# Optimization experiments

Hardware: AMD Instinct MI355X
Metric: run time of the kernel (lower is better)

Reference implementation:

```python
import jax, jax.numpy as jnp
import numpy as np

B, T, I, H = 2048, 1024, 1, 64


def setup_inputs() -> dict:
    key = jax.random.key(0)
    ks = jax.random.split(key, 7)
    s = 1.0 / np.sqrt(H)
    return {
        "x": jax.random.normal(ks[0], (B, T, I), dtype=jnp.float32),
        "W_ih": jax.random.uniform(ks[1], (H, I), jnp.float32, -s, s),
        "W_hh": jax.random.uniform(ks[2], (H, H), jnp.float32, -s, s),
        "b_ih": jax.random.uniform(ks[3], (H,), jnp.float32, -s, s),
        "b_hh": jax.random.uniform(ks[4], (H,), jnp.float32, -s, s),
        "W_out": jax.random.uniform(ks[5], (1, H), jnp.float32, -s, s),
        "b_out": jax.random.uniform(ks[6], (1,), jnp.float32, -s, s),
    }


def reference(x, W_ih, W_hh, b_ih, b_hh, W_out, b_out):
    # x: [B, T, I] -> time-major [T, B, I]
    xt = jnp.swapaxes(x, 0, 1)
    # precompute input projection for all timesteps: [T, B, H]
    xp = jnp.einsum('tbi,hi->tbh', xt, W_ih) + b_ih + b_hh
    h0 = jnp.zeros((x.shape[0], W_hh.shape[0]), dtype=x.dtype)

    def step(h, xp_t):
        h_new = jnp.tanh(xp_t + h @ W_hh.T)
        return h_new, None

    h_last, _ = jax.lax.scan(step, h0, xp)
    # final linear + sigmoid on last timestep: [B, 1]
    return jax.nn.sigmoid(h_last @ W_out.T + b_out)
```

## Files before the change

kernel.cpp:

```cpp
#include <hip/hip_runtime.h>


constexpr int T_STEPS = 1024;
constexpr int H = 64;

typedef float v2f __attribute__((ext_vector_type(2)));
typedef float v4f __attribute__((ext_vector_type(4)));

__device__ __forceinline__ float dpp_rotfwd_add(float t, float a) {
    int y = __builtin_amdgcn_mov_dpp(__builtin_bit_cast(int, t), 0x39, 0xF, 0xF, true);
    return __builtin_bit_cast(float, y) + a;
}

__device__ __forceinline__ float tanh_fast(float s) {
    const float e = __builtin_amdgcn_exp2f(s * 2.88539008177792681472f);
    return 1.f - 2.f * __builtin_amdgcn_rcpf(e + 1.f);
}

__global__
__attribute__((amdgpu_flat_work_group_size(64, 64), amdgpu_waves_per_eu(2, 2)))
void rnn_fused(
    const float* __restrict__ x,
    const float* __restrict__ W_ih,
    const float* __restrict__ W_hh,
    const float* __restrict__ b_ih,
    const float* __restrict__ b_hh,
    const float* __restrict__ W_out,
    const float* __restrict__ b_out,
    float* __restrict__ out)
{
    const int b    = blockIdx.x;
    const int lane = threadIdx.x;
    const int og   = lane >> 2;
    const int kg   = lane & 3;

    __shared__ v4f xs4[T_STEPS / 4];
    __shared__ v4f hA4[H / 4];
    __shared__ v4f hB4[H / 4];

    const v4f* xrow = reinterpret_cast<const v4f*>(x + (size_t)b * T_STEPS);
    #pragma unroll
    for (int k = 0; k < T_STEPS / 4 / 64; ++k)
        xs4[lane + 64 * k] = xrow[lane + 64 * k];

    v2f w2[4][8];
    #pragma unroll
    for (int r = 0; r < 4; ++r) {
        const int row = 4 * og + ((kg + r) & 3);
        const float* src = W_hh + (size_t)row * H + 16 * kg;
        #pragma unroll
        for (int c2 = 0; c2 < 8; ++c2)
            w2[r][c2] = *reinterpret_cast<const v2f*>(src + 2 * c2);
    }
    #pragma unroll
    for (int r = 0; r < 4; ++r)
        #pragma unroll
        for (int c2 = 0; c2 < 8; ++c2)
            asm volatile("" : "+v"(w2[r][c2]));

    const float wih  = W_ih[lane];
    const float bias = b_ih[lane] + b_hh[lane];
    const float wout = W_out[lane];

    reinterpret_cast<float*>(hA4)[lane] = 0.f;

    float hn = 0.f;

    auto step = [&](float xv, const v4f* __restrict__ hr,
                    float* __restrict__ hw) {
        const v4f* h4 = hr + 4 * kg;
        v2f accL[4], accM[4];
        accL[0] = v2f{fmaf(xv, wih, bias), 0.f};
        accL[1] = v2f{0.f, 0.f}; accL[2] = v2f{0.f, 0.f}; accL[3] = v2f{0.f, 0.f};
        accM[0] = v2f{0.f, 0.f}; accM[1] = v2f{0.f, 0.f};
        accM[2] = v2f{0.f, 0.f}; accM[3] = v2f{0.f, 0.f};
        #pragma unroll
        for (int c = 0; c < 4; ++c) {
            const v4f hv = h4[c];
            const v2f hlo = __builtin_shufflevector(hv, hv, 0, 1);
            const v2f hhi = __builtin_shufflevector(hv, hv, 2, 3);
            #pragma unroll
            for (int r = 0; r < 4; ++r) {
                accL[r] = __builtin_elementwise_fma(hlo, w2[r][2 * c],     accL[r]);
                accM[r] = __builtin_elementwise_fma(hhi, w2[r][2 * c + 1], accM[r]);
            }
        }
        float a[4];
        #pragma unroll
        for (int r = 0; r < 4; ++r) {
            const v2f s2 = accL[r] + accM[r];
            a[r] = s2.x + s2.y;
        }
        float t = a[1];
        t = dpp_rotfwd_add(t, a[2]);
        t = dpp_rotfwd_add(t, a[3]);
        t = dpp_rotfwd_add(t, a[0]);
        hn = tanh_fast(t);
        hw[lane] = hn;
    };

    #pragma unroll 1
    for (int t4 = 0; t4 < T_STEPS / 4; ++t4) {
        const v4f xq = xs4[t4];
        step(xq.x, hA4, reinterpret_cast<float*>(hB4));
        step(xq.y, hB4, reinterpret_cast<float*>(hA4));
        step(xq.z, hA4, reinterpret_cast<float*>(hB4));
        step(xq.w, hB4, reinterpret_cast<float*>(hA4));
    }

    float p = hn * wout;
    #pragma unroll
    for (int off = 1; off <= 32; off <<= 1)
        p += __shfl_xor(p, off);
    if (lane == 0)
        out[b] = 1.f / (1.f + __expf(-(p + b_out[0])));
}

extern "C" void kernel_launch(void* const* d_in, const int* in_sizes, int n_in,
                              void* d_out, int out_size, void* d_ws, size_t ws_size,
                              hipStream_t stream)
{
    const float* x     = (const float*)d_in[0];
    const float* W_ih  = (const float*)d_in[1];
    const float* W_hh  = (const float*)d_in[2];
    const float* b_ih  = (const float*)d_in[3];
    const float* b_hh  = (const float*)d_in[4];
    const float* W_out = (const float*)d_in[5];
    const float* b_out = (const float*)d_in[6];
    float* out = (float*)d_out;

    const int B = out_size;
    rnn_fused<<<B, 64, 0, stream>>>(x, W_ih, W_hh, b_ih, b_hh, W_out, b_out, out);
}
```

Baseline: 234.5 us.

## Interleave two independent batch rows per wave to hide recurrence latency

Each 64-lane workgroup now runs two batch sequences, alternating their timesteps, and the grid is halved. Because the two recurrences are independent, one sequence's LDS reads, FMAs, DPP reduction and tanh can overlap the other's dependency chain. Occupancy is lowered to one wave per EU, and the first FMA round is peeled so it starts from multiplies instead of zeroed accumulators. The trade-off is fewer waves to hide latency and an assumption that B is even.

Result: slower. 256.9 us (+9.5%).

```diff
diff --git a/kernel.cpp b/kernel.cpp
--- a/kernel.cpp
+++ b/kernel.cpp
@@ -17,8 +17,11 @@
     return 1.f - 2.f * __builtin_amdgcn_rcpf(e + 1.f);
 }
 
+__device__ __forceinline__ v2f vlo(v4f v) { return __builtin_shufflevector(v, v, 0, 1); }
+__device__ __forceinline__ v2f vhi(v4f v) { return __builtin_shufflevector(v, v, 2, 3); }
+
 __global__
-__attribute__((amdgpu_flat_work_group_size(64, 64), amdgpu_waves_per_eu(2, 2)))
+__attribute__((amdgpu_flat_work_group_size(64, 64), amdgpu_waves_per_eu(1, 1)))
 void rnn_fused(
     const float* __restrict__ x,
     const float* __restrict__ W_ih,
@@ -29,19 +32,23 @@
     const float* __restrict__ b_out,
     float* __restrict__ out)
 {
-    const int b    = blockIdx.x;
+    const int bid  = blockIdx.x;
     const int lane = threadIdx.x;
     const int og   = lane >> 2;
     const int kg   = lane & 3;
 
-    __shared__ v4f xs4[T_STEPS / 4];
-    __shared__ v4f hA4[H / 4];
-    __shared__ v4f hB4[H / 4];
+    __shared__ v4f xsA[T_STEPS / 4];
+    __shared__ v4f xsB[T_STEPS / 4];
+    __shared__ v4f hA0[H / 4], hA1[H / 4];
+    __shared__ v4f hB0[H / 4], hB1[H / 4];
 
-    const v4f* xrow = reinterpret_cast<const v4f*>(x + (size_t)b * T_STEPS);
+    const v4f* xrowA = reinterpret_cast<const v4f*>(x + (size_t)(2 * bid)     * T_STEPS);
+    const v4f* xrowB = reinterpret_cast<const v4f*>(x + (size_t)(2 * bid + 1) * T_STEPS);
     #pragma unroll
-    for (int k = 0; k < T_STEPS / 4 / 64; ++k)
-        xs4[lane + 64 * k] = xrow[lane + 64 * k];
+    for (int k = 0; k < T_STEPS / 4 / 64; ++k) {
+        xsA[lane + 64 * k] = xrowA[lane + 64 * k];
+        xsB[lane + 64 * k] = xrowB[lane + 64 * k];
+    }
 
     v2f w2[4][8];
     #pragma unroll
@@ -62,28 +69,37 @@
     const float bias = b_ih[lane] + b_hh[lane];
     const float wout = W_out[lane];
 
-    reinterpret_cast<float*>(hA4)[lane] = 0.f;
-
-    float hn = 0.f;
+    reinterpret_cast<float*>(hA0)[lane] = 0.f;
+    reinterpret_cast<float*>(hB0)[lane] = 0.f;
 
     auto step = [&](float xv, const v4f* __restrict__ hr,
-                    float* __restrict__ hw) {
+                    float* __restrict__ hw) -> float {
         const v4f* h4 = hr + 4 * kg;
+        const v4f hv0 = h4[0], hv1 = h4[1], hv2 = h4[2], hv3 = h4[3];
+        const float seed = fmaf(xv, wih, bias);
         v2f accL[4], accM[4];
-        accL[0] = v2f{fmaf(xv, wih, bias), 0.f};
-        accL[1] = v2f{0.f, 0.f}; accL[2] = v2f{0.f, 0.f}; accL[3] = v2f{0.f, 0.f};
-        accM[0] = v2f{0.f, 0.f}; accM[1] = v2f{0.f, 0.f};
-        accM[2] = v2f{0.f, 0.f}; accM[3] = v2f{0.f, 0.f};
+        accL[0] = __builtin_elementwise_fma(vlo(hv0), w2[0][0], v2f{seed, 0.f});
+        accL[1] = vlo(hv0) * w2[1][0];
+        accL[2] = vlo(hv0) * w2[2][0];
+        accL[3] = vlo(hv0) * w2[3][0];
+        accM[0] = vhi(hv0) * w2[0][1];
+        accM[1] = vhi(hv0) * w2[1][1];
+        accM[2] = vhi(hv0) * w2[2][1];
+        accM[3] = vhi(hv0) * w2[3][1];
         #pragma unroll
-        for (int c = 0; c < 4; ++c) {
-            const v4f hv = h4[c];
-            const v2f hlo = __builtin_shufflevector(hv, hv, 0, 1);
-            const v2f hhi = __builtin_shufflevector(hv, hv, 2, 3);
-            #pragma unroll
-            for (int r = 0; r < 4; ++r) {
-                accL[r] = __builtin_elementwise_fma(hlo, w2[r][2 * c],     accL[r]);
-                accM[r] = __builtin_elementwise_fma(hhi, w2[r][2 * c + 1], accM[r]);
-            }
+        for (int r = 0; r < 4; ++r) {
+            accL[r] = __builtin_elementwise_fma(vlo(hv1), w2[r][2], accL[r]);
+            accM[r] = __builtin_elementwise_fma(vhi(hv1), w2[r][3], accM[r]);
+        }
+        #pragma unroll
+        for (int r = 0; r < 4; ++r) {
+            accL[r] = __builtin_elementwise_fma(vlo(hv2), w2[r][4], accL[r]);
+            accM[r] = __builtin_elementwise_fma(vhi(hv2), w2[r][5], accM[r]);
+        }
+        #pragma unroll
+        for (int r = 0; r < 4; ++r) {
+            accL[r] = __builtin_elementwise_fma(vlo(hv3), w2[r][6], accL[r]);
+            accM[r] = __builtin_elementwise_fma(vhi(hv3), w2[r][7], accM[r]);
         }
         float a[4];
         #pragma unroll
@@ -95,25 +111,38 @@
         t = dpp_rotfwd_add(t, a[2]);
         t = dpp_rotfwd_add(t, a[3]);
         t = dpp_rotfwd_add(t, a[0]);
-        hn = tanh_fast(t);
+        const float hn = tanh_fast(t);
         hw[lane] = hn;
+        return hn;
     };
 
+    float hnA = 0.f, hnB = 0.f;
     #pragma unroll 1
     for (int t4 = 0; t4 < T_STEPS / 4; ++t4) {
-        const v4f xq = xs4[t4];
-        step(xq.x, hA4, reinterpret_cast<float*>(hB4));
-        step(xq.y, hB4, reinterpret_cast<float*>(hA4));
-        step(xq.z, hA4, reinterpret_cast<float*>(hB4));
-        step(xq.w, hB4, reinterpret_cast<float*>(hA4));
+        const v4f xqA = xsA[t4];
+        const v4f xqB = xsB[t4];
+        hnA = step(xqA.x, hA0, reinterpret_cast<float*>(hA1));
+        hnB = step(xqB.x, hB0, reinterpret_cast<float*>(hB1));
+        hnA = step(xqA.y, hA1, reinterpret_cast<float*>(hA0));
+        hnB = step(xqB.y, hB1, reinterpret_cast<float*>(hB0));
+        hnA = step(xqA.z, hA0, reinterpret_cast<float*>(hA1));
+        hnB = step(xqB.z, hB0, reinterpret_cast<float*>(hB1));
+        hnA = step(xqA.w, hA1, reinterpret_cast<float*>(hA0));
+        hnB = step(xqB.w, hB1, reinterpret_cast<float*>(hB0));
     }
 
-    float p = hn * wout;
+    float pA = hnA * wout;
+    float pB = hnB * wout;
     #pragma unroll
-    for (int off = 1; off <= 32; off <<= 1)
-        p += __shfl_xor(p, off);
-    if (lane == 0)
-        out[b] = 1.f / (1.f + __expf(-(p + b_out[0])));
+    for (int off = 1; off <= 32; off <<= 1) {
+        pA += __shfl_xor(pA, off);
+        pB += __shfl_xor(pB, off);
+    }
+    if (lane == 0) {
+        const float bo = b_out[0];
+        out[2 * bid]     = 1.f / (1.f + __expf(-(pA + bo)));
+        out[2 * bid + 1] = 1.f / (1.f + __expf(-(pB + bo)));
+    }
 }
 
 extern "C" void kernel_launch(void* const* d_in, const int* in_sizes, int n_in,
@@ -130,5 +159,5 @@
     float* out = (float*)d_out;
 
     const int B = out_size;
-    rnn_fused<<<B, 64, 0, stream>>>(x, W_ih, W_hh, b_ih, b_hh, W_out, b_out, out);
+    rnn_fused<<<B / 2, 64, 0, stream>>>(x, W_ih, W_hh, b_ih, b_hh, W_out, b_out, out);
 }
```

## Exchange hidden state via DPP row rotations instead of LDS round-trips

Applied to the files above, without the earlier changes.

The hidden state now stays in registers. Each step broadcasts it with DPP row-rotate moves and reduces partial sums with ds_swizzle and a cross-half shuffle, replacing the per-step LDS write and vector reads. The weight registers are re-laid out in a permuted index mapping so the rotations line up with the stored weights. This aims to remove LDS latency from the serial recurrence critical path, at the cost of many DPP movs per step plus a swizzle and a bpermute-based shuffle that also carry latency.

New measurement: 273.5 us. 16.6% more time.

```diff
diff --git a/kernel.cpp b/kernel.cpp
--- a/kernel.cpp
+++ b/kernel.cpp
@@ -7,9 +7,24 @@
 typedef float v2f __attribute__((ext_vector_type(2)));
 typedef float v4f __attribute__((ext_vector_type(4)));
 
-__device__ __forceinline__ float dpp_rotfwd_add(float t, float a) {
-    int y = __builtin_amdgcn_mov_dpp(__builtin_bit_cast(int, t), 0x39, 0xF, 0xF, true);
-    return __builtin_bit_cast(float, y) + a;
+template <int CTRL>
+__device__ __forceinline__ float dpp_movf(float x) {
+    return __builtin_bit_cast(float,
+        __builtin_amdgcn_mov_dpp(__builtin_bit_cast(int, x), CTRL, 0xF, 0xF, true));
+}
+
+template <int J>
+__device__ __forceinline__ v2f ror2(v2f p) {
+    constexpr int ctrl = 0x120 + 2 * J;
+    v2f r;
+    r.x = dpp_movf<ctrl>(p.x);
+    r.y = dpp_movf<ctrl>(p.y);
+    return r;
+}
+
+__device__ __forceinline__ float swz16(float x) {
+    return __builtin_bit_cast(float,
+        __builtin_amdgcn_ds_swizzle(__builtin_bit_cast(int, x), 0x401F));
 }
 
 __device__ __forceinline__ float tanh_fast(float s) {
@@ -29,91 +44,87 @@
     const float* __restrict__ b_out,
     float* __restrict__ out)
 {
-    const int b    = blockIdx.x;
+    const int bidx = blockIdx.x;
     const int lane = threadIdx.x;
-    const int og   = lane >> 2;
-    const int kg   = lane & 3;
+    const int a    = lane >> 4;
+    const int bq   = lane & 15;
+    const int pi   = 4 * bq + a;
 
     __shared__ v4f xs4[T_STEPS / 4];
-    __shared__ v4f hA4[H / 4];
-    __shared__ v4f hB4[H / 4];
 
-    const v4f* xrow = reinterpret_cast<const v4f*>(x + (size_t)b * T_STEPS);
+    const v4f* xrow = reinterpret_cast<const v4f*>(x + (size_t)bidx * T_STEPS);
     #pragma unroll
     for (int k = 0; k < T_STEPS / 4 / 64; ++k)
         xs4[lane + 64 * k] = xrow[lane + 64 * k];
 
     v2f w2[4][8];
     #pragma unroll
-    for (int r = 0; r < 4; ++r) {
-        const int row = 4 * og + ((kg + r) & 3);
-        const float* src = W_hh + (size_t)row * H + 16 * kg;
+    for (int s = 0; s < 4; ++s) {
+        const int o = 4 * bq + (s ^ a);
+        const float* wr = W_hh + (size_t)o * H;
         #pragma unroll
-        for (int c2 = 0; c2 < 8; ++c2)
-            w2[r][c2] = *reinterpret_cast<const v2f*>(src + 2 * c2);
+        for (int j = 0; j < 8; ++j) {
+            const int c = (bq - 2 * j) & 15;
+            w2[s][j] = v2f{wr[4 * c + a], wr[4 * (c ^ 1) + a]};
+        }
     }
     #pragma unroll
-    for (int r = 0; r < 4; ++r)
+    for (int s = 0; s < 4; ++s)
         #pragma unroll
-        for (int c2 = 0; c2 < 8; ++c2)
-            asm volatile("" : "+v"(w2[r][c2]));
+        for (int j = 0; j < 8; ++j)
+            asm volatile("" : "+v"(w2[s][j]));
 
-    const float wih  = W_ih[lane];
-    const float bias = b_ih[lane] + b_hh[lane];
-    const float wout = W_out[lane];
-
-    reinterpret_cast<float*>(hA4)[lane] = 0.f;
+    const float wihp  = W_ih[pi];
+    const float biasp = b_ih[pi] + b_hh[pi];
+    const float woutp = W_out[pi];
 
     float hn = 0.f;
 
-    auto step = [&](float xv, const v4f* __restrict__ hr,
-                    float* __restrict__ hw) {
-        const v4f* h4 = hr + 4 * kg;
-        v2f accL[4], accM[4];
-        accL[0] = v2f{fmaf(xv, wih, bias), 0.f};
-        accL[1] = v2f{0.f, 0.f}; accL[2] = v2f{0.f, 0.f}; accL[3] = v2f{0.f, 0.f};
-        accM[0] = v2f{0.f, 0.f}; accM[1] = v2f{0.f, 0.f};
-        accM[2] = v2f{0.f, 0.f}; accM[3] = v2f{0.f, 0.f};
-        #pragma unroll
-        for (int c = 0; c < 4; ++c) {
-            const v4f hv = h4[c];
-            const v2f hlo = __builtin_shufflevector(hv, hv, 0, 1);
-            const v2f hhi = __builtin_shufflevector(hv, hv, 2, 3);
-            #pragma unroll
-            for (int r = 0; r < 4; ++r) {
-                accL[r] = __builtin_elementwise_fma(hlo, w2[r][2 * c],     accL[r]);
-                accM[r] = __builtin_elementwise_fma(hhi, w2[r][2 * c + 1], accM[r]);
-            }
+    auto step = [&](float xv) {
+        const float seed = fmaf(xv, wihp, biasp);
+        v2f p0;
+        p0.x = hn;
+        p0.y = dpp_movf<0xB1>(hn);
+        v2f acc0 = __builtin_elementwise_fma(p0, w2[0][0], v2f{seed, 0.f});
+        v2f acc1 = p0 * w2[1][0];
+        v2f acc2 = p0 * w2[2][0];
+        v2f acc3 = p0 * w2[3][0];
+        #define ROT_ACC(J)                                                  \
+        {                                                                   \
+            const v2f pj = ror2<J>(p0);                                     \
+            acc0 = __builtin_elementwise_fma(pj, w2[0][J], acc0);           \
+            acc1 = __builtin_elementwise_fma(pj, w2[1][J], acc1);           \
+            acc2 = __builtin_elementwise_fma(pj, w2[2][J], acc2);           \
+            acc3 = __builtin_elementwise_fma(pj, w2[3][J], acc3);           \
         }
-        float a[4];
-        #pragma unroll
-        for (int r = 0; r < 4; ++r) {
-            const v2f s2 = accL[r] + accM[r];
-            a[r] = s2.x + s2.y;
-        }
-        float t = a[1];
-        t = dpp_rotfwd_add(t, a[2]);
-        t = dpp_rotfwd_add(t, a[3]);
-        t = dpp_rotfwd_add(t, a[0]);
+        ROT_ACC(1) ROT_ACC(2) ROT_ACC(3) ROT_ACC(4)
+        ROT_ACC(5) ROT_ACC(6) ROT_ACC(7)
+        #undef ROT_ACC
+        const float m0 = acc0.x + acc0.y;
+        const float m1 = acc1.x + acc1.y;
+        const float m2 = acc2.x + acc2.y;
+        const float m3 = acc3.x + acc3.y;
+        const float r0 = m0 + swz16(m1);
+        const float r2 = m2 + swz16(m3);
+        const float t = r0 + __shfl_xor(r2, 32);
         hn = tanh_fast(t);
-        hw[lane] = hn;
     };
 
     #pragma unroll 1
     for (int t4 = 0; t4 < T_STEPS / 4; ++t4) {
         const v4f xq = xs4[t4];
-        step(xq.x, hA4, reinterpret_cast<float*>(hB4));
-        step(xq.y, hB4, reinterpret_cast<float*>(hA4));
-        step(xq.z, hA4, reinterpret_cast<float*>(hB4));
-        step(xq.w, hB4, reinterpret_cast<float*>(hA4));
+        step(xq.x);
+        step(xq.y);
+        step(xq.z);
+        step(xq.w);
     }
 
-    float p = hn * wout;
+    float p = hn * woutp;
     #pragma unroll
     for (int off = 1; off <= 32; off <<= 1)
         p += __shfl_xor(p, off);
     if (lane == 0)
-        out[b] = 1.f / (1.f + __expf(-(p + b_out[0])));
+        out[bidx] = 1.f / (1.f + __expf(-(p + b_out[0])));
 }
 
 extern "C" void kernel_launch(void* const* d_in, const int* in_sizes, int n_in,
```
